# Kernel tuning notes

Hardware: AMD Instinct MI355X
Metric: run time of the kernel (lower is better)

The kernel has to match this reference:

```python
import jax, jax.numpy as jnp
import numpy as np

B = 1024
IN_SIZ = 16384
OUT_SIZ = 16384
C = 8          # channel_siz
NLVL = 10
IFS = IN_SIZ // 2 ** NLVL                                   # 16, in_filter_siz
KLVL = min(int(np.floor(np.log2(OUT_SIZ / 2))), NLVL)       # 10
OFS = OUT_SIZ // 2 ** KLVL                                  # 16, out_filter_siz
STD = 0.9


def setup_inputs() -> dict:
    key = jax.random.key(0)
    ks = jax.random.split(key, 2 * NLVL + 3)
    inp = {}
    inp["x"] = jax.random.normal(ks[0], (B, IN_SIZ, 1), jnp.float32)
    inp["in_filter"] = jax.random.normal(ks[1], (IFS, 1, C), jnp.float32) * STD
    inp["in_bias"] = jnp.zeros((C,), jnp.float32)
    for lvl in range(1, NLVL + 1):
        k = 2 ** lvl
        inp[f"W{lvl}"] = jax.random.normal(ks[2 * lvl], (k, 2, C, C), jnp.float32) * STD
        inp[f"b{lvl}"] = jnp.zeros((k, C), jnp.float32)
    inp["fea_dense"] = jax.random.normal(ks[-1], (2 ** KLVL, C, OFS), jnp.float32) * STD
    return inp


def _level(v, W, b):
    # v: [Kp, B, L, C] parent branches; W: [2*Kp, 2, C, C]; b: [2*Kp, C]
    # kernel-2 stride-2 conv1d: out[t] = relu(x[2t] @ W[0] + x[2t+1] @ W[1] + b)
    Kp, Bn, L, Cc = v.shape
    xp = v.reshape(Kp, Bn, L // 2, 2, Cc)
    xr = jnp.repeat(xp, 2, axis=0)  # child itk reads parent itk // 2
    y = jnp.einsum('kbtsc,kscd->kbtd', xr, W) + b[:, None, None, :]
    return jax.nn.relu(y)


def reference(x, in_filter, in_bias,
              W1, b1, W2, b2, W3, b3, W4, b4, W5, b5,
              W6, b6, W7, b7, W8, b8, W9, b9, W10, b10,
              fea_dense):
    Ws = [W1, W2, W3, W4, W5, W6, W7, W8, W9, W10]
    bs = [b1, b2, b3, b4, b5, b6, b7, b8, b9, b10]
    Bn = x.shape[0]
    # input conv1d: kernel=IFS, stride=IFS (non-overlapping) == blocked matmul
    xin = x[..., 0].reshape(Bn, 2 ** NLVL, IFS)                       # [B, 1024, 16]
    v = jax.nn.relu(jnp.einsum('bnf,fc->bnc', xin, in_filter[:, 0, :]) + in_bias)
    v = v[None]                                                        # [1, B, 1024, C]
    for lvl in range(NLVL):  # klvl == nlvl: all levels branch (tree doubling)
        v = _level(v, Ws[lvl], bs[lvl])
    # v: [2^klvl, B, 1, C] -> per-branch dense feature map
    out = jnp.einsum('kbc,kcf->bkf', v[:, :, 0, :], fea_dense)         # [B, 1024, OFS]
    return out.reshape(Bn, OUT_SIZ, 1)
```

## Files before the change

kernel.cpp:

```cpp
#include <hip/hip_runtime.h>

struct PrepPtrs { const float* W[7]; const float* Bv[7]; const float* F; const float* fb; };

__device__ __forceinline__ int cz(int c) { return c ^ ((c >> 3) & 3); }

__device__ __forceinline__ float4 relu4(float4 a) {
  return make_float4(fmaxf(a.x,0.f), fmaxf(a.y,0.f), fmaxf(a.z,0.f), fmaxf(a.w,0.f));
}
__device__ __forceinline__ void fma4(float4& acc, float s, const float4& wv) {
  acc.x = fmaf(s, wv.x, acc.x); acc.y = fmaf(s, wv.y, acc.y);
  acc.z = fmaf(s, wv.z, acc.z); acc.w = fmaf(s, wv.w, acc.w);
}

__global__ void bfly_prep(PrepPtrs P, float* __restrict__ wt) {
  int e = blockIdx.x * 256 + threadIdx.x;
  if (e >= 510 * 68) return;
  int ent = e / 68, r = e % 68, dd = r & 3;
  float v; int dst;
  if (ent < 62) {
    dst = ent * 80 + r;
    if (ent < 60) {
      int lvl, base;
      if (ent < 4)       { lvl = 1; base = 0;  }
      else if (ent < 12) { lvl = 2; base = 4;  }
      else if (ent < 28) { lvl = 3; base = 12; }
      else               { lvl = 4; base = 28; }
      int k = (ent - base) >> 1, th = ent & 1;
      if (r < 64) { int s = r >> 5, c = (r >> 2) & 7;
        v = P.W[lvl-1][k*128 + s*64 + c*8 + th*4 + dd]; }
      else v = P.Bv[lvl-1][k*8 + th*4 + dd];
    } else {
      int th = ent - 60;
      if (r < 64) { int f = r >> 2; v = P.F[f*8 + th*4 + dd]; }
      else v = P.fb[th*4 + dd];
    }
  } else {
    int eb = ent - 62;
    int q = eb / 56, rem = eb % 56;
    int lvl, Kl, base;
    if (rem < 8)       { lvl = 5; Kl = 4;  base = 0;  }
    else if (rem < 24) { lvl = 6; Kl = 8;  base = 8;  }
    else               { lvl = 7; Kl = 16; base = 24; }
    int rr = rem - base, lk = rr >> 1, th = rr & 1;
    int kg = q * Kl + lk;
    if (r < 64) { int s = r >> 5, c = (r >> 2) & 7;
      v = P.W[lvl-1][kg*128 + s*64 + c*8 + th*4 + dd]; }
    else v = P.Bv[lvl-1][kg*8 + th*4 + dd];
    dst = 4960 + eb * 80 + r;
  }
  wt[dst] = v;
}

template<int L>
__device__ __forceinline__ void ka_level(const float4* __restrict__ src,
                                         float4* __restrict__ dst,
                                         const float4* __restrict__ wt4,
                                         int lane, int wq, int th) {
  constexpr int Kc = 1 << L, Tc = 1024 >> L;
  constexpr int entBase = (Kc - 2) * 2;
  constexpr int kIters = (L <= 2) ? 1 : (1 << (L - 2));
  constexpr int tIters = 4 / kIters;
#pragma unroll
  for (int ik = 0; ik < kIters; ++ik) {
    int k;
    if constexpr (L == 1) k = wq & 1;
    else if constexpr (L == 2) k = wq;
    else k = wq + 4 * ik;
    const float4* e4 = wt4 + (entBase + k * 2 + th) * 20;
    const int kp = k >> 1;
#pragma unroll
    for (int it = 0; it < tIters; ++it) {
      int t;
      if constexpr (L == 1) t = lane + (wq >> 1) * 64 + it * 128;
      else if constexpr (L == 2) t = lane + it * 64;
      else if constexpr (L == 3) t = lane + it * 64;
      else t = lane;
      int pb = kp * (2 * Tc) + 2 * t;
      float4 A0 = src[cz(pb)],        C0 = src[cz(pb + 1)];
      float4 A1 = src[cz(pb + 1024)], C1 = src[cz(pb + 1025)];
      float4 a = e4[16];
      fma4(a, A0.x, e4[0]);  fma4(a, A0.y, e4[1]);  fma4(a, A0.z, e4[2]);  fma4(a, A0.w, e4[3]);
      fma4(a, A1.x, e4[4]);  fma4(a, A1.y, e4[5]);  fma4(a, A1.z, e4[6]);  fma4(a, A1.w, e4[7]);
      fma4(a, C0.x, e4[8]);  fma4(a, C0.y, e4[9]);  fma4(a, C0.z, e4[10]); fma4(a, C0.w, e4[11]);
      fma4(a, C1.x, e4[12]); fma4(a, C1.y, e4[13]); fma4(a, C1.z, e4[14]); fma4(a, C1.w, e4[15]);
      dst[cz(th * 1024 + k * Tc + t)] = relu4(a);
    }
  }
}

__global__ __launch_bounds__(512, 2) void bfly_ka(
    const float* __restrict__ x, const float* __restrict__ wt,
    float* __restrict__ st1)
{
  __shared__ float4 sA[2048], sB[2048];
  const int tid = threadIdx.x, b = blockIdx.x;
  const int lane = tid & 63;
  const int wv = __builtin_amdgcn_readfirstlane(tid >> 6);
  const int th = wv & 1, wq = wv >> 1;
  const float4* wt4 = (const float4*)wt;

  {
    const float4* e4 = wt4 + (60 + th) * 20;
    const float* xb = x + (size_t)b * 16384;
#pragma unroll
    for (int i = 0; i < 4; ++i) {
      int n = lane + wq * 64 + i * 256;
      const float4* xr = (const float4*)(xb + n * 16);
      float4 x0 = xr[0], x1 = xr[1], x2 = xr[2], x3 = xr[3];
      float4 a = e4[16];
      fma4(a, x0.x, e4[0]);  fma4(a, x0.y, e4[1]);  fma4(a, x0.z, e4[2]);  fma4(a, x0.w, e4[3]);
      fma4(a, x1.x, e4[4]);  fma4(a, x1.y, e4[5]);  fma4(a, x1.z, e4[6]);  fma4(a, x1.w, e4[7]);
      fma4(a, x2.x, e4[8]);  fma4(a, x2.y, e4[9]);  fma4(a, x2.z, e4[10]); fma4(a, x2.w, e4[11]);
      fma4(a, x3.x, e4[12]); fma4(a, x3.y, e4[13]); fma4(a, x3.z, e4[14]); fma4(a, x3.w, e4[15]);
      sA[cz(th * 1024 + n)] = relu4(a);
    }
  }
  __syncthreads();
  ka_level<1>(sA, sB, wt4, lane, wq, th); __syncthreads();
  ka_level<2>(sB, sA, wt4, lane, wq, th); __syncthreads();
  ka_level<3>(sA, sB, wt4, lane, wq, th); __syncthreads();
  ka_level<4>(sB, sA, wt4, lane, wq, th); __syncthreads();

  float4* o4 = (float4*)st1;
#pragma unroll
  for (int it = 0; it < 4; ++it) {
    int o = tid + it * 512;
    int t4 = o & 63, k4 = (o >> 6) & 15, h = o >> 10;
    o4[((size_t)(h * 16 + k4) * 1024 + b) * 64 + t4] = sA[cz(o)];
  }
}

template<int LV>
__device__ __forceinline__ void kb_level(const float4* __restrict__ src,
                                         float4* __restrict__ dst,
                                         const float4* __restrict__ wb4,
                                         int lane, int wv) {
  constexpr int Kc = 1 << (LV - 3);
  constexpr int Tc = 128 / Kc;
  constexpr int Tp = 256 / Kc;
  constexpr int entB = (LV == 5) ? 0 : (LV == 6) ? 8 : 24;
  constexpr int kIters = Kc / 4;
  constexpr int nIt = 4 / kIters;
  const int th = wv & 1, w2 = wv >> 1;
#pragma unroll
  for (int ik = 0; ik < kIters; ++ik) {
    const int lk = w2 + 4 * ik;
    const float4* e4 = wb4 + (entB + lk * 2 + th) * 20;
    const int lkp = lk >> 1;
#pragma unroll
    for (int it = 0; it < nIt; ++it) {
      int t, bb;
      if constexpr (LV == 5)      { t = lane & 31; bb = (lane >> 5) + it * 2; }
      else if constexpr (LV == 6) { t = lane & 15; bb = (lane >> 4) + it * 4; }
      else                        { t = lane & 7;  bb = lane >> 3; }
      int pb = bb * 256 + lkp * Tp + 2 * t;
      float4 A0 = src[cz(pb)],       C0 = src[cz(pb + 1)];
      float4 A1 = src[cz(pb + 128)], C1 = src[cz(pb + 129)];
      float4 a = e4[16];
      fma4(a, A0.x, e4[0]);  fma4(a, A0.y, e4[1]);  fma4(a, A0.z, e4[2]);  fma4(a, A0.w, e4[3]);
      fma4(a, A1.x, e4[4]);  fma4(a, A1.y, e4[5]);  fma4(a, A1.z, e4[6]);  fma4(a, A1.w, e4[7]);
      fma4(a, C0.x, e4[8]);  fma4(a, C0.y, e4[9]);  fma4(a, C0.z, e4[10]); fma4(a, C0.w, e4[11]);
      fma4(a, C1.x, e4[12]); fma4(a, C1.y, e4[13]); fma4(a, C1.z, e4[14]); fma4(a, C1.w, e4[15]);
      dst[cz(bb * 256 + th * 128 + lk * Tc + t)] = relu4(a);
    }
  }
}

__global__ __launch_bounds__(512, 2) void bfly_kb(
    const float* __restrict__ st1, const float* __restrict__ wt,
    float* __restrict__ st2)
{
  __shared__ float4 s0[2048], s1[2048];
  const int tid = threadIdx.x;
  const int q = blockIdx.x, bt = blockIdx.y;
  const int lane = tid & 63;
  const int wv = __builtin_amdgcn_readfirstlane(tid >> 6);
  const float4* wb4 = (const float4*)wt + 1240 + q * 56 * 20;
  const float4* i4 = (const float4*)st1;

#pragma unroll
  for (int it = 0; it < 4; ++it) {
    int o = tid + it * 512;
    int t4 = o & 63, lk4 = (o >> 6) & 1, h = (o >> 7) & 1, bl = o >> 8;
    float4 v = i4[((size_t)(h * 16 + 2 * q + lk4) * 1024 + bt * 8 + bl) * 64 + t4];
    s0[cz(bl * 256 + h * 128 + lk4 * 64 + t4)] = v;
  }
  __syncthreads();
  kb_level<5>(s0, s1, wb4, lane, wv); __syncthreads();
  kb_level<6>(s1, s0, wb4, lane, wv); __syncthreads();
  kb_level<7>(s0, s1, wb4, lane, wv); __syncthreads();

  float4* o4 = (float4*)st2;
#pragma unroll
  for (int it = 0; it < 4; ++it) {
    int o = tid + it * 512;
    int bl = o & 7, t7 = (o >> 3) & 7, h = (o >> 6) & 1, lk7 = o >> 7;
    float4 v = s1[cz(bl * 256 + h * 128 + lk7 * 8 + t7)];
    o4[((size_t)((16 * q + lk7) * 8 + t7) * 2 + h) * 1024 + bt * 8 + bl] = v;
  }
}

struct Wmat {
  float4 w0,w1,w2,w3,w4,w5,w6,w7,w8,w9,w10,w11,w12,w13,w14,w15,b;
};
__device__ __forceinline__ Wmat loadWm(const float* __restrict__ swt,
                                       int woff, int boff, int k_l, int th) {
  Wmat m;
  const float4* p = (const float4*)(swt + woff + k_l * 128 + th * 4);
  m.w0 = p[0];  m.w1 = p[2];  m.w2 = p[4];  m.w3 = p[6];
  m.w4 = p[8];  m.w5 = p[10]; m.w6 = p[12]; m.w7 = p[14];
  m.w8 = p[16]; m.w9 = p[18]; m.w10 = p[20]; m.w11 = p[22];
  m.w12 = p[24]; m.w13 = p[26]; m.w14 = p[28]; m.w15 = p[30];
  m.b = *(const float4*)(swt + boff + k_l * 8 + th * 4);
  return m;
}
__device__ __forceinline__ float4 matApply(const Wmat& m, float4 A0, float4 A1,
                                           float4 C0, float4 C1) {
  float4 a = m.b;
  fma4(a, A0.x, m.w0);  fma4(a, A0.y, m.w1);  fma4(a, A0.z, m.w2);  fma4(a, A0.w, m.w3);
  fma4(a, A1.x, m.w4);  fma4(a, A1.y, m.w5);  fma4(a, A1.z, m.w6);  fma4(a, A1.w, m.w7);
  fma4(a, C0.x, m.w8);  fma4(a, C0.y, m.w9);  fma4(a, C0.z, m.w10); fma4(a, C0.w, m.w11);
  fma4(a, C1.x, m.w12); fma4(a, C1.y, m.w13); fma4(a, C1.z, m.w14); fma4(a, C1.w, m.w15);
  return relu4(a);
}

__global__ __launch_bounds__(512, 2) void bfly_kc(
    const float* __restrict__ st,
    const float* __restrict__ W8, const float* __restrict__ B8,
    const float* __restrict__ W9, const float* __restrict__ B9,
    const float* __restrict__ W10, const float* __restrict__ B10,
    const float* __restrict__ fea, float* __restrict__ out)
{
  __shared__ float4 sA[1024], sB[1024];
  __shared__ float swt[2928];
  const int tid = threadIdx.x;
  const int j = blockIdx.x, b0 = blockIdx.y * 64;
  const int bb = tid & 63, grp = tid >> 6;

  {
    const float4* s4 = (const float4*)st;
#pragma unroll
    for (int it = 0; it < 2; ++it) {
      int idx = tid + it * 512;
      int bl = idx & 63, h = (idx >> 6) & 1, t = idx >> 7;
      sA[h * 512 + t * 64 + bl] = s4[((size_t)((j * 8 + t) * 2 + h)) * 1024 + b0 + bl];
    }
  }
  {
    float4* d = (float4*)swt;
    for (int i = tid; i < 64;  i += 512) d[i]       = ((const float4*)(W8  + j*256 ))[i];
    for (int i = tid; i < 128; i += 512) d[64+i]    = ((const float4*)(W9  + j*512 ))[i];
    for (int i = tid; i < 256; i += 512) d[192+i]   = ((const float4*)(W10 + j*1024))[i];
    if (tid < 4)  d[448+tid] = ((const float4*)(B8  + j*16))[tid];
    if (tid < 8)  d[452+tid] = ((const float4*)(B9  + j*32))[tid];
    if (tid < 16) d[460+tid] = ((const float4*)(B10 + j*64))[tid];
    for (int i = tid; i < 256; i += 512) d[476+i]   = ((const float4*)(fea + j*1024))[i];
  }
  __syncthreads();

  {
    int h = grp >> 2, k = (grp >> 1) & 1, ti = grp & 1;
    Wmat m = loadWm(swt, 0, 1792, k, h);
#pragma unroll
    for (int i = 0; i < 2; ++i) {
      int t = ti + 2 * i;
      float4 A0 = sA[(2*t) * 64 + bb],     A1 = sA[512 + (2*t) * 64 + bb];
      float4 C0 = sA[(2*t+1) * 64 + bb],   C1 = sA[512 + (2*t+1) * 64 + bb];
      sB[h * 512 + (2*t + k) * 64 + bb] = matApply(m, A0, A1, C0, C1);
    }
  }
  __syncthreads();
  {
    int h = grp >> 2, k9 = grp & 3;
    Wmat m = loadWm(swt, 256, 1808, k9, h);
#pragma unroll
    for (int t9 = 0; t9 < 2; ++t9) {
      int p0 = 4 * t9 + (k9 >> 1), p1 = p0 + 2;
      float4 A0 = sB[p0 * 64 + bb], A1 = sB[512 + p0 * 64 + bb];
      float4 C0 = sB[p1 * 64 + bb], C1 = sB[512 + p1 * 64 + bb];
      sA[h * 512 + (t9 * 4 + k9) * 64 + bb] = matApply(m, A0, A1, C0, C1);
    }
  }
  __syncthreads();
  {
    int k10 = grp;
    int p0 = k10 >> 1, p1 = p0 + 4;
    float4 A0 = sA[p0 * 64 + bb], A1 = sA[512 + p0 * 64 + bb];
    float4 C0 = sA[p1 * 64 + bb], C1 = sA[512 + p1 * 64 + bb];
#pragma unroll 1
    for (int h = 0; h < 2; ++h) {
      Wmat m = loadWm(swt, 768, 1840, k10, h);
      sB[h * 512 + k10 * 64 + bb] = matApply(m, A0, A1, C0, C1);
    }
  }
  __syncthreads();
  {
    int cc = tid & 31, bgrp = tid >> 5;
    int k = cc >> 2, fq = cc & 3;
    const float* fp = swt + 1904 + k * 128 + fq * 4;
    float4 f0 = *(const float4*)(fp);        float4 f1 = *(const float4*)(fp + 16);
    float4 f2 = *(const float4*)(fp + 32);   float4 f3 = *(const float4*)(fp + 48);
    float4 f4_ = *(const float4*)(fp + 64);  float4 f5 = *(const float4*)(fp + 80);
    float4 f6 = *(const float4*)(fp + 96);   float4 f7 = *(const float4*)(fp + 112);
#pragma unroll
    for (int it = 0; it < 4; ++it) {
      int b_l = bgrp + it * 16;
      float4 s0v = sB[k * 64 + b_l];
      float4 s1v = sB[512 + k * 64 + b_l];
      float4 acc = make_float4(0.f, 0.f, 0.f, 0.f);
      fma4(acc, s0v.x, f0);  fma4(acc, s0v.y, f1);
      fma4(acc, s0v.z, f2);  fma4(acc, s0v.w, f3);
      fma4(acc, s1v.x, f4_); fma4(acc, s1v.y, f5);
      fma4(acc, s1v.z, f6);  fma4(acc, s1v.w, f7);
      *(float4*)(out + ((size_t)(b0 + b_l)) * 16384 + j * 128 + k * 16 + fq * 4) = acc;
    }
  }
}

extern "C" void kernel_launch(void* const* d_in, const int* in_sizes, int n_in,
                              void* d_out, int out_size, void* d_ws, size_t ws_size,
                              hipStream_t stream) {
  const float* x  = (const float*)d_in[0];
  PrepPtrs P;
  P.F  = (const float*)d_in[1];
  P.fb = (const float*)d_in[2];
  for (int l = 0; l < 7; ++l) {
    P.W[l]  = (const float*)d_in[3 + 2 * l];
    P.Bv[l] = (const float*)d_in[4 + 2 * l];
  }
  const float* W8  = (const float*)d_in[17];
  const float* B8  = (const float*)d_in[18];
  const float* W9  = (const float*)d_in[19];
  const float* B9  = (const float*)d_in[20];
  const float* W10 = (const float*)d_in[21];
  const float* B10 = (const float*)d_in[22];
  const float* fea = (const float*)d_in[23];
  float* wt  = (float*)d_ws;
  float* st2 = (float*)d_ws + 65536;
  float* st1 = (float*)d_out;
  float* out = (float*)d_out;

  bfly_prep<<<dim3(136), dim3(256), 0, stream>>>(P, wt);
  bfly_ka<<<dim3(1024), dim3(512), 0, stream>>>(x, wt, st1);
  bfly_kb<<<dim3(8, 128), dim3(512), 0, stream>>>(st1, wt, st2);
  bfly_kc<<<dim3(128, 16), dim3(512), 0, stream>>>(st2, W8, B8, W9, B9, W10, B10, fea, out);
}
```

Before: 97.35 us.

## Prepack levels 8-10 weights in prep kernel and read them wave-uniformly in kc

The prep kernel now also repacks W8-W10 and their biases into the workspace in the per-(k,half) 80-float entry layout already used for earlier levels, and the staging buffer offset moves to make room. The final kernel drops its shared-memory weight staging and the sync that followed it. Each wave now reads its matrix entry directly from global memory through a wave-uniform (readfirstlane) pointer, so the loads can become scalar loads. Each wave now covers two work items per level. The fea matrix is also read straight from global memory. This cuts LDS use and a load-and-sync phase, in exchange for more prep work and a dependence on scalar and L1 cache hits.

```diff
diff --git a/kernel.cpp b/kernel.cpp
--- a/kernel.cpp
+++ b/kernel.cpp
@@ -1,6 +1,10 @@
 #include <hip/hip_runtime.h>
 
-struct PrepPtrs { const float* W[7]; const float* Bv[7]; const float* F; const float* fb; };
+struct PrepPtrs {
+  const float* W[7]; const float* Bv[7]; const float* F; const float* fb;
+  const float* W8; const float* B8; const float* W9; const float* B9;
+  const float* W10; const float* B10;
+};
 
 __device__ __forceinline__ int cz(int c) { return c ^ ((c >> 3) & 3); }
 
@@ -14,41 +18,45 @@
 
 __global__ void bfly_prep(PrepPtrs P, float* __restrict__ wt) {
   int e = blockIdx.x * 256 + threadIdx.x;
-  if (e >= 510 * 68) return;
+  if (e >= 4094 * 68) return;
   int ent = e / 68, r = e % 68, dd = r & 3;
-  float v; int dst;
+  const float* Ws; const float* Bs; int th;
   if (ent < 62) {
-    dst = ent * 80 + r;
     if (ent < 60) {
       int lvl, base;
       if (ent < 4)       { lvl = 1; base = 0;  }
       else if (ent < 12) { lvl = 2; base = 4;  }
       else if (ent < 28) { lvl = 3; base = 12; }
       else               { lvl = 4; base = 28; }
-      int k = (ent - base) >> 1, th = ent & 1;
-      if (r < 64) { int s = r >> 5, c = (r >> 2) & 7;
-        v = P.W[lvl-1][k*128 + s*64 + c*8 + th*4 + dd]; }
-      else v = P.Bv[lvl-1][k*8 + th*4 + dd];
+      int k = (ent - base) >> 1; th = ent & 1;
+      Ws = P.W[lvl-1] + k*128; Bs = P.Bv[lvl-1] + k*8;
     } else {
-      int th = ent - 60;
-      if (r < 64) { int f = r >> 2; v = P.F[f*8 + th*4 + dd]; }
-      else v = P.fb[th*4 + dd];
-    }
-  } else {
+      th = ent - 60; Ws = P.F; Bs = P.fb;
+    }
+  } else if (ent < 510) {
     int eb = ent - 62;
     int q = eb / 56, rem = eb % 56;
     int lvl, Kl, base;
     if (rem < 8)       { lvl = 5; Kl = 4;  base = 0;  }
     else if (rem < 24) { lvl = 6; Kl = 8;  base = 8;  }
     else               { lvl = 7; Kl = 16; base = 24; }
-    int rr = rem - base, lk = rr >> 1, th = rr & 1;
+    int rr = rem - base; int lk = rr >> 1; th = rr & 1;
     int kg = q * Kl + lk;
-    if (r < 64) { int s = r >> 5, c = (r >> 2) & 7;
-      v = P.W[lvl-1][kg*128 + s*64 + c*8 + th*4 + dd]; }
-    else v = P.Bv[lvl-1][kg*8 + th*4 + dd];
-    dst = 4960 + eb * 80 + r;
-  }
-  wt[dst] = v;
+    Ws = P.W[lvl-1] + kg*128; Bs = P.Bv[lvl-1] + kg*8;
+  } else if (ent < 1022) {
+    int ec = ent - 510; int k = ec >> 1; th = ec & 1;
+    Ws = P.W8 + k*128; Bs = P.B8 + k*8;
+  } else if (ent < 2046) {
+    int ec = ent - 1022; int k = ec >> 1; th = ec & 1;
+    Ws = P.W9 + k*128; Bs = P.B9 + k*8;
+  } else {
+    int ec = ent - 2046; int k = ec >> 1; th = ec & 1;
+    Ws = P.W10 + k*128; Bs = P.B10 + k*8;
+  }
+  float v;
+  if (r < 64) { int s = r >> 5, c = (r >> 2) & 7; v = Ws[s*64 + c*8 + th*4 + dd]; }
+  else v = Bs[th*4 + dd];
+  wt[ent * 80 + r] = v;
 }
 
 template<int L>
@@ -200,42 +208,16 @@
   }
 }
 
-struct Wmat {
-  float4 w0,w1,w2,w3,w4,w5,w6,w7,w8,w9,w10,w11,w12,w13,w14,w15,b;
-};
-__device__ __forceinline__ Wmat loadWm(const float* __restrict__ swt,
-                                       int woff, int boff, int k_l, int th) {
-  Wmat m;
-  const float4* p = (const float4*)(swt + woff + k_l * 128 + th * 4);
-  m.w0 = p[0];  m.w1 = p[2];  m.w2 = p[4];  m.w3 = p[6];
-  m.w4 = p[8];  m.w5 = p[10]; m.w6 = p[12]; m.w7 = p[14];
-  m.w8 = p[16]; m.w9 = p[18]; m.w10 = p[20]; m.w11 = p[22];
-  m.w12 = p[24]; m.w13 = p[26]; m.w14 = p[28]; m.w15 = p[30];
-  m.b = *(const float4*)(swt + boff + k_l * 8 + th * 4);
-  return m;
-}
-__device__ __forceinline__ float4 matApply(const Wmat& m, float4 A0, float4 A1,
-                                           float4 C0, float4 C1) {
-  float4 a = m.b;
-  fma4(a, A0.x, m.w0);  fma4(a, A0.y, m.w1);  fma4(a, A0.z, m.w2);  fma4(a, A0.w, m.w3);
-  fma4(a, A1.x, m.w4);  fma4(a, A1.y, m.w5);  fma4(a, A1.z, m.w6);  fma4(a, A1.w, m.w7);
-  fma4(a, C0.x, m.w8);  fma4(a, C0.y, m.w9);  fma4(a, C0.z, m.w10); fma4(a, C0.w, m.w11);
-  fma4(a, C1.x, m.w12); fma4(a, C1.y, m.w13); fma4(a, C1.z, m.w14); fma4(a, C1.w, m.w15);
-  return relu4(a);
-}
-
 __global__ __launch_bounds__(512, 2) void bfly_kc(
-    const float* __restrict__ st,
-    const float* __restrict__ W8, const float* __restrict__ B8,
-    const float* __restrict__ W9, const float* __restrict__ B9,
-    const float* __restrict__ W10, const float* __restrict__ B10,
+    const float* __restrict__ st, const float* __restrict__ wt,
     const float* __restrict__ fea, float* __restrict__ out)
 {
   __shared__ float4 sA[1024], sB[1024];
-  __shared__ float swt[2928];
   const int tid = threadIdx.x;
   const int j = blockIdx.x, b0 = blockIdx.y * 64;
-  const int bb = tid & 63, grp = tid >> 6;
+  const int bb = tid & 63;
+  const int w = __builtin_amdgcn_readfirstlane(tid >> 6);
+  const float4* wt4 = (const float4*)wt;
 
   {
     const float4* s4 = (const float4*)st;
@@ -246,58 +228,53 @@
       sA[h * 512 + t * 64 + bl] = s4[((size_t)((j * 8 + t) * 2 + h)) * 1024 + b0 + bl];
     }
   }
-  {
-    float4* d = (float4*)swt;
-    for (int i = tid; i < 64;  i += 512) d[i]       = ((const float4*)(W8  + j*256 ))[i];
-    for (int i = tid; i < 128; i += 512) d[64+i]    = ((const float4*)(W9  + j*512 ))[i];
-    for (int i = tid; i < 256; i += 512) d[192+i]   = ((const float4*)(W10 + j*1024))[i];
-    if (tid < 4)  d[448+tid] = ((const float4*)(B8  + j*16))[tid];
-    if (tid < 8)  d[452+tid] = ((const float4*)(B9  + j*32))[tid];
-    if (tid < 16) d[460+tid] = ((const float4*)(B10 + j*64))[tid];
-    for (int i = tid; i < 256; i += 512) d[476+i]   = ((const float4*)(fea + j*1024))[i];
-  }
-  __syncthreads();
-
-  {
-    int h = grp >> 2, k = (grp >> 1) & 1, ti = grp & 1;
-    Wmat m = loadWm(swt, 0, 1792, k, h);
-#pragma unroll
-    for (int i = 0; i < 2; ++i) {
-      int t = ti + 2 * i;
-      float4 A0 = sA[(2*t) * 64 + bb],     A1 = sA[512 + (2*t) * 64 + bb];
-      float4 C0 = sA[(2*t+1) * 64 + bb],   C1 = sA[512 + (2*t+1) * 64 + bb];
-      sB[h * 512 + (2*t + k) * 64 + bb] = matApply(m, A0, A1, C0, C1);
-    }
-  }
-  __syncthreads();
-  {
-    int h = grp >> 2, k9 = grp & 3;
-    Wmat m = loadWm(swt, 256, 1808, k9, h);
-#pragma unroll
-    for (int t9 = 0; t9 < 2; ++t9) {
-      int p0 = 4 * t9 + (k9 >> 1), p1 = p0 + 2;
-      float4 A0 = sB[p0 * 64 + bb], A1 = sB[512 + p0 * 64 + bb];
-      float4 C0 = sB[p1 * 64 + bb], C1 = sB[512 + p1 * 64 + bb];
-      sA[h * 512 + (t9 * 4 + k9) * 64 + bb] = matApply(m, A0, A1, C0, C1);
-    }
-  }
-  __syncthreads();
-  {
-    int k10 = grp;
+  __syncthreads();
+
+  auto mat = [&](const float4* e4, float4 A0, float4 A1, float4 C0, float4 C1) {
+    float4 a = e4[16];
+    fma4(a, A0.x, e4[0]);  fma4(a, A0.y, e4[1]);  fma4(a, A0.z, e4[2]);  fma4(a, A0.w, e4[3]);
+    fma4(a, A1.x, e4[4]);  fma4(a, A1.y, e4[5]);  fma4(a, A1.z, e4[6]);  fma4(a, A1.w, e4[7]);
+    fma4(a, C0.x, e4[8]);  fma4(a, C0.y, e4[9]);  fma4(a, C0.z, e4[10]); fma4(a, C0.w, e4[11]);
+    fma4(a, C1.x, e4[12]); fma4(a, C1.y, e4[13]); fma4(a, C1.z, e4[14]); fma4(a, C1.w, e4[15]);
+    return relu4(a);
+  };
+
+#pragma unroll
+  for (int ii = 0; ii < 2; ++ii) {
+    int s = w + ii * 8;
+    int th = s >> 3, k = (s >> 2) & 1, t = s & 3;
+    const float4* e4 = wt4 + (510 + (2 * j + k) * 2 + th) * 20;
+    float4 A0 = sA[(2*t) * 64 + bb],   A1 = sA[512 + (2*t) * 64 + bb];
+    float4 C0 = sA[(2*t+1) * 64 + bb], C1 = sA[512 + (2*t+1) * 64 + bb];
+    sB[th * 512 + (2*t + k) * 64 + bb] = mat(e4, A0, A1, C0, C1);
+  }
+  __syncthreads();
+#pragma unroll
+  for (int ii = 0; ii < 2; ++ii) {
+    int s = w + ii * 8;
+    int th = s >> 3, k9 = (s >> 1) & 3, t9 = s & 1;
+    const float4* e4 = wt4 + (1022 + (4 * j + k9) * 2 + th) * 20;
+    int p0 = 4 * t9 + (k9 >> 1), p1 = p0 + 2;
+    float4 A0 = sB[p0 * 64 + bb], A1 = sB[512 + p0 * 64 + bb];
+    float4 C0 = sB[p1 * 64 + bb], C1 = sB[512 + p1 * 64 + bb];
+    sA[th * 512 + (t9 * 4 + k9) * 64 + bb] = mat(e4, A0, A1, C0, C1);
+  }
+  __syncthreads();
+#pragma unroll
+  for (int ii = 0; ii < 2; ++ii) {
+    int s = w + ii * 8;
+    int th = s >> 3, k10 = s & 7;
+    const float4* e4 = wt4 + (2046 + (8 * j + k10) * 2 + th) * 20;
     int p0 = k10 >> 1, p1 = p0 + 4;
     float4 A0 = sA[p0 * 64 + bb], A1 = sA[512 + p0 * 64 + bb];
     float4 C0 = sA[p1 * 64 + bb], C1 = sA[512 + p1 * 64 + bb];
-#pragma unroll 1
-    for (int h = 0; h < 2; ++h) {
-      Wmat m = loadWm(swt, 768, 1840, k10, h);
-      sB[h * 512 + k10 * 64 + bb] = matApply(m, A0, A1, C0, C1);
-    }
+    sB[th * 512 + k10 * 64 + bb] = mat(e4, A0, A1, C0, C1);
   }
   __syncthreads();
   {
     int cc = tid & 31, bgrp = tid >> 5;
     int k = cc >> 2, fq = cc & 3;
-    const float* fp = swt + 1904 + k * 128 + fq * 4;
+    const float* fp = fea + (size_t)(j * 8 + k) * 128 + fq * 4;
     float4 f0 = *(const float4*)(fp);        float4 f1 = *(const float4*)(fp + 16);
     float4 f2 = *(const float4*)(fp + 32);   float4 f3 = *(const float4*)(fp + 48);
     float4 f4_ = *(const float4*)(fp + 64);  float4 f5 = *(const float4*)(fp + 80);
@@ -328,20 +305,20 @@
     P.W[l]  = (const float*)d_in[3 + 2 * l];
     P.Bv[l] = (const float*)d_in[4 + 2 * l];
   }
-  const float* W8  = (const float*)d_in[17];
-  const float* B8  = (const float*)d_in[18];
-  const float* W9  = (const float*)d_in[19];
-  const float* B9  = (const float*)d_in[20];
-  const float* W10 = (const float*)d_in[21];
-  const float* B10 = (const float*)d_in[22];
+  P.W8  = (const float*)d_in[17];
+  P.B8  = (const float*)d_in[18];
+  P.W9  = (const float*)d_in[19];
+  P.B9  = (const float*)d_in[20];
+  P.W10 = (const float*)d_in[21];
+  P.B10 = (const float*)d_in[22];
   const float* fea = (const float*)d_in[23];
   float* wt  = (float*)d_ws;
-  float* st2 = (float*)d_ws + 65536;
+  float* st2 = (float*)d_ws + 393216;
   float* st1 = (float*)d_out;
   float* out = (float*)d_out;
 
-  bfly_prep<<<dim3(136), dim3(256), 0, stream>>>(P, wt);
+  bfly_prep<<<dim3(1088), dim3(256), 0, stream>>>(P, wt);
   bfly_ka<<<dim3(1024), dim3(512), 0, stream>>>(x, wt, st1);
   bfly_kb<<<dim3(8, 128), dim3(512), 0, stream>>>(st1, wt, st2);
-  bfly_kc<<<dim3(128, 16), dim3(512), 0, stream>>>(st2, W8, B8, W9, B9, W10, B10, fea, out);
-}
+  bfly_kc<<<dim3(128, 16), dim3(512), 0, stream>>>(st2, wt, fea, out);
+}
```

After: 93.04 us. -4.4%, faster.
